# Kernel optimization log

Measured on AMD Instinct MI355X. Metric: run time of the kernel, lower is better.

Reference implementation:

```python
import jax, jax.numpy as jnp
import numpy as np

MARGIN = 2.0
N_STREAM = 4
BRANCH_WEIGHT = np.ones(N_STREAM, dtype=np.float32)  # default branch_weight = [1.0]*n_stream
ALPHA = 1.0 / N_STREAM  # MultistreamLoss default alpha
BETA = 1.0              # MultistreamLoss default beta
EPS = 1e-4


def _ranking(preds, labels):
    # sum over pairs i<j of relu(-(p[j]-p[i]) * sign(l[j]-l[i]) + margin)
    n = preds.shape[0]
    d = preds[None, :] - preds[:, None]          # d[i, j] = p[j] - p[i]
    s = jnp.sign(labels[None, :] - labels[:, None])
    h = jax.nn.relu(-d * s + MARGIN)             # [n, n]
    mask = jnp.triu(jnp.ones((n, n), dtype=bool), k=1)  # j > i
    return jnp.sum(jnp.where(mask, h, jnp.zeros((), h.dtype)))


def setup_inputs() -> dict:
    key = jax.random.key(0)
    k1, k2, k3 = jax.random.split(key, 3)
    n = 4096
    scores = jax.random.normal(k1, (N_STREAM, n), dtype=jnp.float32)
    pred = jax.random.normal(k2, (n,), dtype=jnp.float32)
    label = jax.random.normal(k3, (n,), dtype=jnp.float32)
    return {"scores": scores, "pred": pred, "label": label}


def reference(scores, pred, label):
    # branch ranking losses, one per stream
    branch = jax.vmap(lambda s: _ranking(s, label))(scores)       # [N_STREAM]
    branch_loss = jnp.sum(jnp.asarray(BRANCH_WEIGHT) * branch)

    # BatchRankingMSE_Loss (alpha=None -> 1.0, beta=None -> grad-norm ratio, no renorm)
    mse = jnp.mean((pred - label) ** 2)
    rank = _ranking(pred, label)
    g1 = jnp.linalg.norm(jax.grad(lambda p: jnp.mean((p - label) ** 2))(pred))
    g2 = jnp.linalg.norm(jax.grad(lambda p: _ranking(p, label))(pred))
    beta_w = jax.lax.stop_gradient(g1 / (g2 + EPS))  # computed under no_grad in torch
    pred_loss = 1.0 * mse + beta_w * rank

    return ALPHA * branch_loss + BETA * pred_loss
```

## Files before the change

### kernel.cpp

```cpp
#include <hip/hip_runtime.h>
#include <math.h>

#define N 4096
#define MARGINF 2.0f
#define EPSF 1e-4f
#define SCOPE_AGENT __HIP_MEMORY_SCOPE_AGENT

typedef _Float16 f16x2 __attribute__((ext_vector_type(2)));

__device__ __forceinline__ unsigned f2u(f16x2 h){ return __builtin_bit_cast(unsigned, h); }
__device__ __forceinline__ f16x2 u2f(unsigned u){ return __builtin_bit_cast(f16x2, u); }
__device__ __forceinline__ unsigned pku(float a, float b){
    return __builtin_bit_cast(unsigned, __builtin_amdgcn_cvt_pkrtz(a, b));
}
__device__ __forceinline__ f16x2 pk2(float a){ return u2f(pku(a, a)); }
__device__ __forceinline__ float fdot2(f16x2 a, f16x2 b, float c){
    return __builtin_amdgcn_fdot2(a, b, c, false);
}
__device__ __forceinline__ f16x2 c_one(){ return u2f(0x3C003C00u); }
__device__ __forceinline__ f16x2 c_two(){ return u2f(0x40004000u); }
__device__ __forceinline__ f16x2 c_zero(){ return u2f(0u); }
__device__ __forceinline__ f16x2 c_big(){ return u2f(0x7BFF7BFFu); }

constexpr int CC = 128;
constexpr int SCORE_PER_STREAM = 80;
constexpr int NPRED_BLK = 128;
constexpr int NSCORE_BLK = 4 * SCORE_PER_STREAM;
constexpr int NPROD = NPRED_BLK + NSCORE_BLK;
constexpr int RTS = 1024;

constexpr int CTR_OFF = 0;
constexpr int A_OFF   = 64;
constexpr int B_OFF   = 640;
constexpr int C_OFF   = 832;

__device__ __forceinline__ void body2(unsigned lm2u, unsigned pm2u,
                                      f16x2 lk2, f16x2 rk2, float& acc){
    const f16x2 ld2 = u2f(lm2u) - lk2;
    const unsigned sgn = f2u(ld2) & 0x80008000u;
    const f16x2 pd2 = u2f(pm2u) - rk2;
    const f16x2 x2 = u2f(f2u(pd2) ^ sgn);
    const f16x2 m2 = __builtin_elementwise_max(c_two() - x2, c_zero());
    acc = fdot2(m2, c_one(), acc);
}

__device__ __forceinline__ void body2m(unsigned lm2u, unsigned pm2u,
                                       f16x2 lk2, f16x2 rk2, int d, float& acc){
    const f16x2 ld2 = u2f(lm2u) - lk2;
    const unsigned sgn = f2u(ld2) & 0x80008000u;
    const f16x2 pd2 = u2f(pm2u) - rk2;
    const f16x2 x2 = u2f(f2u(pd2) ^ sgn);
    const f16x2 m2 = __builtin_elementwise_max(c_two() - x2, c_zero());
    const unsigned mu = (d >= 0) ? ((d > 0) ? 0x3C003C00u : 0x3C000000u) : 0u;
    acc = fdot2(m2, u2f(mu), acc);
}

__device__ __forceinline__ void body2g(unsigned lm2u, unsigned pm2u,
                                       f16x2 lk2, f16x2 rk2, float& acc, float& gacc){
    const f16x2 ld2 = u2f(lm2u) - lk2;
    const unsigned sgn = f2u(ld2) & 0x80008000u;
    const f16x2 pd2 = u2f(pm2u) - rk2;
    const f16x2 x2 = u2f(f2u(pd2) ^ sgn);
    const f16x2 m2 = __builtin_elementwise_max(c_two() - x2, c_zero());
    acc = fdot2(m2, c_one(), acc);
    const f16x2 ind2 = __builtin_elementwise_min(m2 * c_big(), c_one());
    gacc = fdot2(u2f(f2u(ind2) ^ sgn), c_one(), gacc);
}

__global__ __launch_bounds__(256) void fused_kernel(
    const float* __restrict__ scores, const float* __restrict__ pred,
    const float* __restrict__ label, float* __restrict__ ws,
    float* __restrict__ out)
{
    __shared__ unsigned shm[2 * 2080];
    __shared__ float red[16];

    unsigned* wsu = (unsigned*)ws;
    const int bid = blockIdx.x;
    const int tid = threadIdx.x;

    if (bid == 0) {
        if (tid == 0) {
            const unsigned snap = __hip_atomic_load(wsu + CTR_OFF, __ATOMIC_RELAXED,
                                                    SCOPE_AGENT);
            unsigned guard = 0;
            while ((__hip_atomic_load(wsu + CTR_OFF, __ATOMIC_RELAXED, SCOPE_AGENT)
                    - snap) < (unsigned)NPROD) {
                __builtin_amdgcn_s_sleep(8);
                if (++guard > (1u << 27)) break;
            }
            __threadfence();
        }
        __syncthreads();

        float br = 0.f, pr = 0.f, g2sq = 0.f, sse = 0.f;
        {
            const int b1 = 1 + tid;
            const float a1 = __uint_as_float(__hip_atomic_load(
                wsu + A_OFF + b1, __ATOMIC_RELAXED, SCOPE_AGENT));
            if (b1 <= NPRED_BLK) pr += a1; else br += a1;
            const int b2 = 257 + tid;
            if (b2 <= NPROD) {
                br += __uint_as_float(__hip_atomic_load(
                    wsu + A_OFF + b2, __ATOMIC_RELAXED, SCOPE_AGENT));
            }
            if (tid < NPRED_BLK) {
                g2sq = __uint_as_float(__hip_atomic_load(
                    wsu + B_OFF + 1 + tid, __ATOMIC_RELAXED, SCOPE_AGENT));
                sse  = __uint_as_float(__hip_atomic_load(
                    wsu + C_OFF + 1 + tid, __ATOMIC_RELAXED, SCOPE_AGENT));
            }
        }
        #pragma unroll
        for (int off = 32; off > 0; off >>= 1) {
            br   += __shfl_xor(br,   off, 64);
            pr   += __shfl_xor(pr,   off, 64);
            g2sq += __shfl_xor(g2sq, off, 64);
            sse  += __shfl_xor(sse,  off, 64);
        }
        const int wid = tid >> 6;
        const int lane = tid & 63;
        if (lane == 0) {
            red[wid] = br; red[4 + wid] = pr;
            red[8 + wid] = g2sq; red[12 + wid] = sse;
        }
        __syncthreads();
        if (tid == 0) {
            const float brT   = red[0] + red[1] + red[2] + red[3];
            const float prT   = red[4] + red[5] + red[6] + red[7];
            const float g2sqT = red[8] + red[9] + red[10] + red[11];
            const float sseT  = red[12] + red[13] + red[14] + red[15];
            const float rankp = (prT - (float)N * MARGINF) * 0.5f;
            const float mse = sseT / (float)N;
            const float g1 = (2.0f / (float)N) * sqrtf(sseT);
            const float g2 = sqrtf(g2sqT);
            const float beta = g1 / (g2 + EPSF);
            out[0] = 0.25f * brT + mse + beta * rankp;
        }
        return;
    }

    const bool isPred = (bid <= NPRED_BLK);
    float rank_total, g2sq_total = 0.f, sse_total = 0.f;

    if (isPred) {
        const int rb = (bid - 1) * 32;
        #pragma unroll
        for (int q = 0; q < 8; ++q) {
            const int j = q * 256 + tid;
            const float2 lf = *(const float2*)&label[2 * j];
            shm[q * 260 + tid] = pku(lf.x, lf.y);
            const float2 pf = *(const float2*)&pred[2 * j];
            shm[2080 + q * 260 + tid] = pku(pf.x, pf.y);
        }
        __syncthreads();

        const int rowofs = tid >> 3;
        const int cg = tid & 7;
        const int r = rb + rowofs;
        const f16x2 rk2 = pk2(pred[r]);
        const f16x2 lk2 = pk2(label[r]);
        const unsigned base = cg * 260;

        float acc0 = 0.f, acc1 = 0.f, g0 = 0.f, g1v = 0.f;
        #pragma unroll 4
        for (int it = 0; it < 64; ++it) {
            const uint4 l4 = *(const uint4*)&shm[base + it * 4];
            const uint4 s4 = *(const uint4*)&shm[2080 + base + it * 4];
            body2g(l4.x, s4.x, lk2, rk2, acc0, g0);
            body2g(l4.y, s4.y, lk2, rk2, acc1, g1v);
            body2g(l4.z, s4.z, lk2, rk2, acc0, g0);
            body2g(l4.w, s4.w, lk2, rk2, acc1, g1v);
        }
        rank_total = acc0 + acc1;
        float g = g0 + g1v;
        if (cg == (r >> 9)) g -= 1.0f;
        g += __shfl_xor(g, 1, 64);
        g += __shfl_xor(g, 2, 64);
        g += __shfl_xor(g, 4, 64);
        if (cg == 0) {
            g2sq_total = g * g;
            const float d = pred[r] - label[r];
            sse_total = d * d;
        }
    } else {
        const int b = bid - 1 - NPRED_BLK;
        const int stream = b / SCORE_PER_STREAM;
        const int t = b % SCORE_PER_STREAM;
        int ti, c;
        if      (t < 32) { ti = 0; c = t; }
        else if (t < 56) { ti = 1; c = 8  + (t - 32); }
        else if (t < 72) { ti = 2; c = 16 + (t - 56); }
        else             { ti = 3; c = 24 + (t - 72); }
        const float* __restrict__ p = scores + stream * N;
        const int c0 = c * CC;
        unsigned* lab16 = shm;
        unsigned* col16 = shm + 2080;

        if (tid < CC / 2) {
            const float2 lf = *(const float2*)&label[c0 + 2 * tid];
            lab16[tid] = pku(lf.x, lf.y);
        } else if (tid < CC) {
            const int q = tid - CC / 2;
            const float2 pf = *(const float2*)&p[c0 + 2 * q];
            col16[q] = pku(pf.x, pf.y);
        }
        __syncthreads();

        const int rb = ti * RTS;
        int r[4]; f16x2 rk2[4], lk2[4];
        #pragma unroll
        for (int k = 0; k < 4; ++k) {
            r[k] = rb + tid + 256 * k;
            rk2[k] = pk2(p[r[k]]);
            lk2[k] = pk2(label[r[k]]);
        }
        float acc[8] = {0.f,0.f,0.f,0.f,0.f,0.f,0.f,0.f};

        if (c >= 8 * (ti + 1)) {
            #pragma unroll 4
            for (int q = 0; q < CC / 8; ++q) {
                const uint4 l4 = *(const uint4*)&lab16[q * 4];
                const uint4 s4 = *(const uint4*)&col16[q * 4];
                #pragma unroll
                for (int k = 0; k < 4; ++k) {
                    body2(l4.x, s4.x, lk2[k], rk2[k], acc[k]);
                    body2(l4.y, s4.y, lk2[k], rk2[k], acc[4 + k]);
                    body2(l4.z, s4.z, lk2[k], rk2[k], acc[k]);
                    body2(l4.w, s4.w, lk2[k], rk2[k], acc[4 + k]);
                }
            }
        } else {
            #pragma unroll 4
            for (int q = 0; q < CC / 8; ++q) {
                const uint4 l4 = *(const uint4*)&lab16[q * 4];
                const uint4 s4 = *(const uint4*)&col16[q * 4];
                const int cb = c0 + q * 8;
                #pragma unroll
                for (int k = 0; k < 4; ++k) {
                    body2m(l4.x, s4.x, lk2[k], rk2[k], cb + 0 - r[k], acc[k]);
                    body2m(l4.y, s4.y, lk2[k], rk2[k], cb + 2 - r[k], acc[4 + k]);
                    body2m(l4.z, s4.z, lk2[k], rk2[k], cb + 4 - r[k], acc[k]);
                    body2m(l4.w, s4.w, lk2[k], rk2[k], cb + 6 - r[k], acc[4 + k]);
                }
            }
        }
        rank_total = (acc[0] + acc[1]) + (acc[2] + acc[3])
                   + (acc[4] + acc[5]) + (acc[6] + acc[7]);
    }

    #pragma unroll
    for (int off = 32; off > 0; off >>= 1) {
        rank_total += __shfl_xor(rank_total, off, 64);
        g2sq_total += __shfl_xor(g2sq_total, off, 64);
        sse_total  += __shfl_xor(sse_total,  off, 64);
    }
    const int wid = tid >> 6;
    const int lane = tid & 63;
    if (lane == 0) {
        red[wid] = rank_total; red[4 + wid] = g2sq_total; red[8 + wid] = sse_total;
    }
    __syncthreads();
    if (tid == 0) {
        const float rankT = red[0] + red[1] + red[2] + red[3];
        __hip_atomic_store(wsu + A_OFF + bid, __float_as_uint(rankT),
                           __ATOMIC_RELAXED, SCOPE_AGENT);
        if (isPred) {
            const float g2T  = red[4] + red[5] + red[6] + red[7];
            const float sseT = red[8] + red[9] + red[10] + red[11];
            __hip_atomic_store(wsu + B_OFF + bid, __float_as_uint(g2T),
                               __ATOMIC_RELAXED, SCOPE_AGENT);
            __hip_atomic_store(wsu + C_OFF + bid, __float_as_uint(sseT),
                               __ATOMIC_RELAXED, SCOPE_AGENT);
        }
        __hip_atomic_fetch_add(wsu + CTR_OFF, 1u, __ATOMIC_RELEASE, SCOPE_AGENT);
    }
}

extern "C" void kernel_launch(void* const* d_in, const int* in_sizes, int n_in,
                              void* d_out, int out_size, void* d_ws, size_t ws_size,
                              hipStream_t stream) {
    const float* scores = (const float*)d_in[0];
    const float* pred   = (const float*)d_in[1];
    const float* label  = (const float*)d_in[2];
    float* ws  = (float*)d_ws;
    float* out = (float*)d_out;

    fused_kernel<<<NPROD + 1, 256, 0, stream>>>(scores, pred, label, ws, out);
}
```

Baseline: 20.10 us.

## Double pred-row blocks and shard completion counter across sixteen slots

Pred blocks now each handle 16 rows with 16 column groups instead of 32 rows with 8, doubling the pred block count to 256 and halving per-block loop length. The shared-memory layout is repadded to 132-word rows to match the new column-group split. The single global completion counter is replaced by 16 strided counters polled by one wave and summed with a shuffle reduction, to cut atomic contention on one address. The trade-off is more blocks launched, an extra shuffle in the gradient reduction, and a more complex wait loop in the reducer block.

```diff
diff --git a/kernel.cpp b/kernel.cpp
--- a/kernel.cpp
+++ b/kernel.cpp
@@ -24,15 +24,16 @@
 
 constexpr int CC = 128;
 constexpr int SCORE_PER_STREAM = 80;
-constexpr int NPRED_BLK = 128;
+constexpr int NPRED_BLK = 256;
 constexpr int NSCORE_BLK = 4 * SCORE_PER_STREAM;
 constexpr int NPROD = NPRED_BLK + NSCORE_BLK;
 constexpr int RTS = 1024;
 
-constexpr int CTR_OFF = 0;
-constexpr int A_OFF   = 64;
-constexpr int B_OFF   = 640;
-constexpr int C_OFF   = 832;
+constexpr int NCTR = 16;
+constexpr int CTR_STRIDE = 16;
+constexpr int A_OFF = 256;
+constexpr int B_OFF = 960;
+constexpr int C_OFF = 1280;
 
 __device__ __forceinline__ void body2(unsigned lm2u, unsigned pm2u,
                                       f16x2 lk2, f16x2 rk2, float& acc){
@@ -72,7 +73,7 @@
     const float* __restrict__ label, float* __restrict__ ws,
     float* __restrict__ out)
 {
-    __shared__ unsigned shm[2 * 2080];
+    __shared__ unsigned shm[2 * 2112];
     __shared__ float red[16];
 
     unsigned* wsu = (unsigned*)ws;
@@ -80,36 +81,39 @@
     const int tid = threadIdx.x;
 
     if (bid == 0) {
-        if (tid == 0) {
-            const unsigned snap = __hip_atomic_load(wsu + CTR_OFF, __ATOMIC_RELAXED,
+        if (tid < 64) {
+            const int k = (tid & 15) * CTR_STRIDE;
+            const unsigned snap = __hip_atomic_load(wsu + k, __ATOMIC_RELAXED,
                                                     SCOPE_AGENT);
             unsigned guard = 0;
-            while ((__hip_atomic_load(wsu + CTR_OFF, __ATOMIC_RELAXED, SCOPE_AGENT)
-                    - snap) < (unsigned)NPROD) {
-                __builtin_amdgcn_s_sleep(8);
-                if (++guard > (1u << 27)) break;
-            }
-            __threadfence();
-        }
-        __syncthreads();
+            while (true) {
+                unsigned delta = __hip_atomic_load(wsu + k, __ATOMIC_RELAXED,
+                                                   SCOPE_AGENT) - snap;
+                #pragma unroll
+                for (int off = 32; off > 0; off >>= 1)
+                    delta += __shfl_xor(delta, off, 64);
+                if (delta == 4u * (unsigned)NPROD) break;
+                if (++guard > (1u << 25)) break;
+                __builtin_amdgcn_s_sleep(4);
+            }
+        }
+        __syncthreads();
+        __threadfence();
 
         float br = 0.f, pr = 0.f, g2sq = 0.f, sse = 0.f;
         {
-            const int b1 = 1 + tid;
-            const float a1 = __uint_as_float(__hip_atomic_load(
-                wsu + A_OFF + b1, __ATOMIC_RELAXED, SCOPE_AGENT));
-            if (b1 <= NPRED_BLK) pr += a1; else br += a1;
-            const int b2 = 257 + tid;
-            if (b2 <= NPROD) {
+            pr = __uint_as_float(__hip_atomic_load(
+                wsu + A_OFF + 1 + tid, __ATOMIC_RELAXED, SCOPE_AGENT));
+            br = __uint_as_float(__hip_atomic_load(
+                wsu + A_OFF + 257 + tid, __ATOMIC_RELAXED, SCOPE_AGENT));
+            if (tid < 64) {
                 br += __uint_as_float(__hip_atomic_load(
-                    wsu + A_OFF + b2, __ATOMIC_RELAXED, SCOPE_AGENT));
-            }
-            if (tid < NPRED_BLK) {
-                g2sq = __uint_as_float(__hip_atomic_load(
-                    wsu + B_OFF + 1 + tid, __ATOMIC_RELAXED, SCOPE_AGENT));
-                sse  = __uint_as_float(__hip_atomic_load(
-                    wsu + C_OFF + 1 + tid, __ATOMIC_RELAXED, SCOPE_AGENT));
-            }
+                    wsu + A_OFF + 513 + tid, __ATOMIC_RELAXED, SCOPE_AGENT));
+            }
+            g2sq = __uint_as_float(__hip_atomic_load(
+                wsu + B_OFF + 1 + tid, __ATOMIC_RELAXED, SCOPE_AGENT));
+            sse  = __uint_as_float(__hip_atomic_load(
+                wsu + C_OFF + 1 + tid, __ATOMIC_RELAXED, SCOPE_AGENT));
         }
         #pragma unroll
         for (int off = 32; off > 0; off >>= 1) {
@@ -144,29 +148,30 @@
     float rank_total, g2sq_total = 0.f, sse_total = 0.f;
 
     if (isPred) {
-        const int rb = (bid - 1) * 32;
+        const int rb = (bid - 1) * 16;
         #pragma unroll
         for (int q = 0; q < 8; ++q) {
             const int j = q * 256 + tid;
+            const int addr = (j >> 7) * 132 + (j & 127);
             const float2 lf = *(const float2*)&label[2 * j];
-            shm[q * 260 + tid] = pku(lf.x, lf.y);
+            shm[addr] = pku(lf.x, lf.y);
             const float2 pf = *(const float2*)&pred[2 * j];
-            shm[2080 + q * 260 + tid] = pku(pf.x, pf.y);
-        }
-        __syncthreads();
-
-        const int rowofs = tid >> 3;
-        const int cg = tid & 7;
+            shm[2112 + addr] = pku(pf.x, pf.y);
+        }
+        __syncthreads();
+
+        const int rowofs = tid >> 4;
+        const int cg = tid & 15;
         const int r = rb + rowofs;
         const f16x2 rk2 = pk2(pred[r]);
         const f16x2 lk2 = pk2(label[r]);
-        const unsigned base = cg * 260;
+        const unsigned base = cg * 132;
 
         float acc0 = 0.f, acc1 = 0.f, g0 = 0.f, g1v = 0.f;
         #pragma unroll 4
-        for (int it = 0; it < 64; ++it) {
+        for (int it = 0; it < 32; ++it) {
             const uint4 l4 = *(const uint4*)&shm[base + it * 4];
-            const uint4 s4 = *(const uint4*)&shm[2080 + base + it * 4];
+            const uint4 s4 = *(const uint4*)&shm[2112 + base + it * 4];
             body2g(l4.x, s4.x, lk2, rk2, acc0, g0);
             body2g(l4.y, s4.y, lk2, rk2, acc1, g1v);
             body2g(l4.z, s4.z, lk2, rk2, acc0, g0);
@@ -174,10 +179,11 @@
         }
         rank_total = acc0 + acc1;
         float g = g0 + g1v;
-        if (cg == (r >> 9)) g -= 1.0f;
+        if (cg == (r >> 8)) g -= 1.0f;
         g += __shfl_xor(g, 1, 64);
         g += __shfl_xor(g, 2, 64);
         g += __shfl_xor(g, 4, 64);
+        g += __shfl_xor(g, 8, 64);
         if (cg == 0) {
             g2sq_total = g * g;
             const float d = pred[r] - label[r];
@@ -195,7 +201,7 @@
         const float* __restrict__ p = scores + stream * N;
         const int c0 = c * CC;
         unsigned* lab16 = shm;
-        unsigned* col16 = shm + 2080;
+        unsigned* col16 = shm + 2112;
 
         if (tid < CC / 2) {
             const float2 lf = *(const float2*)&label[c0 + 2 * tid];
@@ -273,7 +279,8 @@
             __hip_atomic_store(wsu + C_OFF + bid, __float_as_uint(sseT),
                                __ATOMIC_RELAXED, SCOPE_AGENT);
         }
-        __hip_atomic_fetch_add(wsu + CTR_OFF, 1u, __ATOMIC_RELEASE, SCOPE_AGENT);
+        __hip_atomic_fetch_add(wsu + (bid & 15) * CTR_STRIDE, 1u,
+                               __ATOMIC_RELEASE, SCOPE_AGENT);
     }
 }
 
```

Measured after the change: 22.43 us. 1.12x slower.
